# Kernel optimization log

Measured on AMD Instinct MI355X. Metric: run time of the kernel, lower is better.

The kernel has to match this reference:

```python
import jax, jax.numpy as jnp
import numpy as np

EPS = 1e-6
N, D = 8192, 256


def setup_inputs() -> dict:
    key = jax.random.key(0)
    kq, kc = jax.random.split(key)
    # scale 0.05 keeps points inside the Poincare ball: c*||q||^2 ~ 0.06 << 1
    query = jax.random.normal(kq, (N, D), dtype=jnp.float32) * 0.05
    c = jnp.asarray(0.1, dtype=jnp.float32)  # learnable curvature param (init 0.1)
    return {"query": query, "c": c}


def reference(query, c):
    # Self-attention path of HyperbolicAttention (keys = values = query).
    clamp_c = jnp.maximum(c, EPS)
    # ||u-v||^2 = ||u||^2 + ||v||^2 - 2 u.v  (same math as explicit expand+subtract,
    # but via a single GEMM instead of an (N, N, D) intermediate)
    qn = jnp.sum(query * query, axis=-1)                       # (N,)
    gram = query @ query.T                                     # (N, N)
    diff_sq = jnp.maximum(qn[:, None] + qn[None, :] - 2.0 * gram, 0.0)
    t = jnp.maximum(1.0 - clamp_c * qn, EPS)                   # clamped 1 - c||x||^2
    denom = t[:, None] * t[None, :]                            # (N, N)
    arg = jnp.maximum(1.0 + 2.0 * clamp_c * diff_sq / denom, 1.0 + EPS) + EPS
    dist = jnp.arccosh(arg) / jnp.sqrt(clamp_c)                # (N, N)
    attn = jax.nn.softmax(-dist, axis=-1)                      # (N, N)
    return attn @ query                                        # (N, D)
```

## Files before the change

### kernel.cpp

```cpp
#include <hip/hip_runtime.h>
#include <math.h>

#define NN 8192
#define DD 256
#define EPSV 1e-6f
#define BM 32
#define BN 256
#define NJT (NN / BN)
#define TSTR 266

typedef __bf16 bf16x8 __attribute__((ext_vector_type(8)));
typedef float f32x16 __attribute__((ext_vector_type(16)));
typedef unsigned short ushort;
typedef unsigned int uint;


__device__ inline ushort f2bf(float x) {
    uint u = __float_as_uint(x);
    u += 0x7fffu + ((u >> 16) & 1u);
    return (ushort)(u >> 16);
}

__global__ void prep_kernel(const float* __restrict__ q, const float* __restrict__ cp,
                            ushort* __restrict__ qbfA, ushort* __restrict__ qbfB,
                            float2* __restrict__ qni) {
    __shared__ ushort T[64 * TSTR];
    const int t = threadIdx.x;
    const int b = blockIdx.x;
    const int pr = t >> 2, fq = t & 3;
    const int row = b * 64 + pr;
    const float4* src = (const float4*)(q + (size_t)row * DD + fq * 64);
    ushort loc[64];
    float ss = 0.f;
    #pragma unroll
    for (int i = 0; i < 16; ++i) {
        float4 v = src[i];
        ushort b0 = f2bf(v.x), b1 = f2bf(v.y), b2 = f2bf(v.z), b3 = f2bf(v.w);
        loc[i * 4 + 0] = b0; loc[i * 4 + 1] = b1; loc[i * 4 + 2] = b2; loc[i * 4 + 3] = b3;
        float r0 = __uint_as_float((uint)b0 << 16), r1 = __uint_as_float((uint)b1 << 16);
        float r2 = __uint_as_float((uint)b2 << 16), r3 = __uint_as_float((uint)b3 << 16);
        ss += r0 * r0 + r1 * r1 + r2 * r2 + r3 * r3;
    }
    #pragma unroll
    for (int k = 0; k < 8; ++k)
        *(uint4*)(qbfA + (((size_t)b * 32 + fq * 8 + k) * 64 + pr) * 8) = *(uint4*)&loc[k * 8];
    #pragma unroll
    for (int k = 0; k < 32; ++k)
        *(ushort2*)&T[pr * TSTR + fq * 64 + k * 2] = *(ushort2*)&loc[k * 2];
    ss += __shfl_xor(ss, 1, 64);
    ss += __shfl_xor(ss, 2, 64);
    if (fq == 0) {
        float cc = fmaxf(cp[0], EPSV);
        float tt = fmaxf(1.0f - cc * ss, EPSV);
        qni[row] = make_float2(ss, sqrtf(2.0f * cc) / tt);
    }
    __syncthreads();
    #pragma unroll
    for (int pass = 0; pass < 4; ++pass) {
        int f = pass * 64 + (t >> 2);
        int quarter = t & 3;
        ushort tmp[16];
        #pragma unroll
        for (int i = 0; i < 16; ++i) tmp[i] = T[(quarter * 16 + i) * TSTR + f];
        *(uint4*)(qbfB + (((size_t)b * 8 + quarter * 2 + 0) * 256 + f) * 8) = *(uint4*)&tmp[0];
        *(uint4*)(qbfB + (((size_t)b * 8 + quarter * 2 + 1) * 256 + f) * 8) = *(uint4*)&tmp[8];
    }
}

__global__ __launch_bounds__(512, 2) void flash_kernel(
    const ushort* __restrict__ qbfA, const ushort* __restrict__ qbfB,
    const float* __restrict__ cp, const float2* __restrict__ qni,
    float* __restrict__ out) {
    __shared__ char px[32768];
    __shared__ float lrow[32];

    const int tid = threadIdx.x;
    const int lane = tid & 63;
    const int w = tid >> 6;
    const int l31 = lane & 31;
    const int lhi = lane >> 5;
    const int bx = blockIdx.x;
    const int R0 = bx * 32;

    if (tid < 32) lrow[tid] = 0.f;

    const float cc = fmaxf(cp[0], EPSV);
    const float nrsc = -rsqrtf(cc);

    bf16x8 qa[16];
    {
        const int jbQ = bx >> 1;
        const int rl = (bx & 1) * 32 + l31;
        #pragma unroll
        for (int kk = 0; kk < 16; ++kk)
            qa[kk] = *(const bf16x8*)(qbfA + (((size_t)jbQ * 32 + kk * 2 + lhi) * 64 + rl) * 8);
    }
    const float2 mv = qni[R0 + l31];
    const float qn_m = mv.x, itv_m = mv.y;

    f32x16 o;
    #pragma unroll
    for (int i = 0; i < 16; ++i) o[i] = 0.f;
    float racc = 0.f;

    #pragma unroll 1
    for (int jt = 0; jt < NJT; ++jt) {
        const int J0 = jt * BN;

        const int jbK = jt * 4 + (w >> 1);
        const int rlK = (w & 1) * 32 + l31;
        f32x16 s;
        #pragma unroll
        for (int i = 0; i < 16; ++i) s[i] = 0.f;
        #pragma unroll
        for (int kk = 0; kk < 16; ++kk) {
            bf16x8 kb = *(const bf16x8*)(qbfA + (((size_t)jbK * 32 + kk * 2 + lhi) * 64 + rlK) * 8);
            s = __builtin_amdgcn_mfma_f32_32x32x16_bf16(kb, qa[kk], s, 0, 0, 0);
        }

        float qnj[16], itj[16];
        #pragma unroll
        for (int rq = 0; rq < 4; ++rq) {
            int j0 = J0 + w * 32 + rq * 8 + 4 * lhi;
            const float4* qp = (const float4*)(qni + j0);
            float4 q01 = qp[0], q23 = qp[1];
            qnj[rq * 4 + 0] = q01.x; itj[rq * 4 + 0] = q01.y;
            qnj[rq * 4 + 1] = q01.z; itj[rq * 4 + 1] = q01.w;
            qnj[rq * 4 + 2] = q23.x; itj[rq * 4 + 2] = q23.y;
            qnj[rq * 4 + 3] = q23.z; itj[rq * 4 + 3] = q23.w;
        }

        float p[16];
        #pragma unroll
        for (int r = 0; r < 16; ++r) {
            float diff = fmaf(-2.0f, s[r], qn_m + qnj[r]);
            float z = fmaf(diff, itv_m * itj[r], 1.0f);
            z = fmaxf(z, 1.0f + EPSV) + EPSV;
            float y = z + sqrtf(fmaf(z, z, -1.0f));
            float pv = __builtin_amdgcn_exp2f(nrsc * __builtin_amdgcn_logf(y));
            racc += pv;
            p[r] = pv;
        }

        float sh[16];
        #pragma unroll
        for (int r = 0; r < 16; ++r) sh[r] = __shfl_xor(p[r], 32, 64);
        bf16x8 af0, af1;
        #pragma unroll
        for (int e = 0; e < 4; ++e) {
            af0[e]     = (__bf16)(lhi ? sh[e + 4]  : p[e]);
            af0[e + 4] = (__bf16)(lhi ? p[e + 4]  : sh[e]);
            af1[e]     = (__bf16)(lhi ? sh[e + 12] : p[e + 8]);
            af1[e + 4] = (__bf16)(lhi ? p[e + 12] : sh[e + 8]);
        }

        char* pxb = px + (jt & 1) * 16384;
        *(bf16x8*)(pxb + (w * 2 + 0) * 1024 + lane * 16) = af0;
        *(bf16x8*)(pxb + (w * 2 + 1) * 1024 + lane * 16) = af1;
        __syncthreads();

        #pragma unroll
        for (int kc = 0; kc < 16; ++kc) {
            bf16x8 pa = *(const bf16x8*)(pxb + kc * 1024 + lane * 16);
            bf16x8 vb = *(const bf16x8*)(qbfB +
                (((size_t)(jt * 16 + kc) * 2 + lhi) * 256 + w * 32 + l31) * 8);
            o = __builtin_amdgcn_mfma_f32_32x32x16_bf16(pa, vb, o, 0, 0, 0);
        }
    }

    racc += __shfl_xor(racc, 32, 64);
    if (lhi == 0) atomicAdd(&lrow[l31], racc);
    __syncthreads();
    #pragma unroll
    for (int r = 0; r < 16; ++r) {
        int row = (r & 3) + 8 * (r >> 2) + 4 * lhi;
        float inv = 1.0f / lrow[row];
        out[(size_t)(R0 + row) * DD + w * 32 + l31] = o[r] * inv;
    }
}

extern "C" void kernel_launch(void* const* d_in, const int* in_sizes, int n_in,
                              void* d_out, int out_size, void* d_ws, size_t ws_size,
                              hipStream_t stream) {
    (void)in_sizes; (void)n_in; (void)out_size; (void)ws_size;
    const float* q = (const float*)d_in[0];
    const float* cp = (const float*)d_in[1];
    float* out = (float*)d_out;
    float* ws = (float*)d_ws;
    float2* qni = (float2*)ws;
    ushort* qbfA = (ushort*)(qni + NN);
    ushort* qbfB = qbfA + (size_t)NN * DD;

    prep_kernel<<<NN / 64, 256, 0, stream>>>(q, cp, qbfA, qbfB, qni);
    flash_kernel<<<NN / BM, 512, 0, stream>>>(qbfA, qbfB, cp, qni, out);
}
```

Measured before the change: 255.7 us.

## Split key dimension across four blocks per row tile with separate normalize kernel

Each row tile's key range is partitioned into four chunks processed by separate blocks. Each block writes its unnormalized output and row sums to workspace, and a new reduction kernel sums them and divides. This is meant to fix underutilization, since there were only 256 blocks before, and launch bounds are raised to allow more blocks per CU. In exchange it adds extra global traffic for the partial results, and the tighter register budget risks spills.

```diff
diff --git a/kernel.cpp b/kernel.cpp
--- a/kernel.cpp
+++ b/kernel.cpp
@@ -6,7 +6,8 @@
 #define EPSV 1e-6f
 #define BM 32
 #define BN 256
-#define NJT (NN / BN)
+#define CSPLIT 4
+#define NJT (NN / CSPLIT / BN)
 #define TSTR 266
 
 typedef __bf16 bf16x8 __attribute__((ext_vector_type(8)));
@@ -67,10 +68,10 @@
     }
 }
 
-__global__ __launch_bounds__(512, 2) void flash_kernel(
+__global__ __launch_bounds__(512, 4) void flash_kernel(
     const ushort* __restrict__ qbfA, const ushort* __restrict__ qbfB,
     const float* __restrict__ cp, const float2* __restrict__ qni,
-    float* __restrict__ out) {
+    float* __restrict__ Oacc, float* __restrict__ lacc) {
     __shared__ char px[32768];
     __shared__ float lrow[32];
 
@@ -79,8 +80,9 @@
     const int w = tid >> 6;
     const int l31 = lane & 31;
     const int lhi = lane >> 5;
-    const int bx = blockIdx.x;
-    const int R0 = bx * 32;
+    const int cs = blockIdx.x & 3;
+    const int rb = blockIdx.x >> 2;
+    const int R0 = rb * BM;
 
     if (tid < 32) lrow[tid] = 0.f;
 
@@ -89,8 +91,8 @@
 
     bf16x8 qa[16];
     {
-        const int jbQ = bx >> 1;
-        const int rl = (bx & 1) * 32 + l31;
+        const int jbQ = rb >> 1;
+        const int rl = (rb & 1) * 32 + l31;
         #pragma unroll
         for (int kk = 0; kk < 16; ++kk)
             qa[kk] = *(const bf16x8*)(qbfA + (((size_t)jbQ * 32 + kk * 2 + lhi) * 64 + rl) * 8);
@@ -105,9 +107,9 @@
 
     #pragma unroll 1
     for (int jt = 0; jt < NJT; ++jt) {
-        const int J0 = jt * BN;
-
-        const int jbK = jt * 4 + (w >> 1);
+        const int J0 = cs * (NN / CSPLIT) + jt * BN;
+
+        const int jbK = (J0 >> 6) + (w >> 1);
         const int rlK = (w & 1) * 32 + l31;
         f32x16 s;
         #pragma unroll
@@ -159,11 +161,12 @@
         *(bf16x8*)(pxb + (w * 2 + 1) * 1024 + lane * 16) = af1;
         __syncthreads();
 
+        const size_t vslot0 = (size_t)(J0 >> 3);
         #pragma unroll
         for (int kc = 0; kc < 16; ++kc) {
             bf16x8 pa = *(const bf16x8*)(pxb + kc * 1024 + lane * 16);
             bf16x8 vb = *(const bf16x8*)(qbfB +
-                (((size_t)(jt * 16 + kc) * 2 + lhi) * 256 + w * 32 + l31) * 8);
+                ((vslot0 + kc * 2 + lhi) * 256 + w * 32 + l31) * 8);
             o = __builtin_amdgcn_mfma_f32_32x32x16_bf16(pa, vb, o, 0, 0, 0);
         }
     }
@@ -171,12 +174,32 @@
     racc += __shfl_xor(racc, 32, 64);
     if (lhi == 0) atomicAdd(&lrow[l31], racc);
     __syncthreads();
+    float* Oslab = Oacc + (size_t)cs * NN * DD;
     #pragma unroll
     for (int r = 0; r < 16; ++r) {
         int row = (r & 3) + 8 * (r >> 2) + 4 * lhi;
-        float inv = 1.0f / lrow[row];
-        out[(size_t)(R0 + row) * DD + w * 32 + l31] = o[r] * inv;
-    }
+        Oslab[(size_t)(R0 + row) * DD + w * 32 + l31] = o[r];
+    }
+    if (tid < 32) lacc[cs * NN + R0 + tid] = lrow[tid];
+}
+
+__global__ void norm_kernel(const float* __restrict__ Oacc, const float* __restrict__ lacc,
+                            float* __restrict__ out) {
+    int i = blockIdx.x * 256 + threadIdx.x;
+    int row = i >> 6;
+    float l = lacc[row] + lacc[NN + row] + lacc[2 * NN + row] + lacc[3 * NN + row];
+    const size_t stride = (size_t)NN * DD / 4;
+    float4 a = ((const float4*)Oacc)[i];
+    float4 b = ((const float4*)Oacc)[i + stride];
+    float4 c = ((const float4*)Oacc)[i + 2 * stride];
+    float4 d = ((const float4*)Oacc)[i + 3 * stride];
+    float inv = 1.0f / l;
+    float4 r;
+    r.x = (a.x + b.x + c.x + d.x) * inv;
+    r.y = (a.y + b.y + c.y + d.y) * inv;
+    r.z = (a.z + b.z + c.z + d.z) * inv;
+    r.w = (a.w + b.w + c.w + d.w) * inv;
+    ((float4*)out)[i] = r;
 }
 
 extern "C" void kernel_launch(void* const* d_in, const int* in_sizes, int n_in,
@@ -190,7 +213,10 @@
     float2* qni = (float2*)ws;
     ushort* qbfA = (ushort*)(qni + NN);
     ushort* qbfB = qbfA + (size_t)NN * DD;
+    float* lacc = (float*)(qbfB + (size_t)NN * DD);
+    float* Oacc = lacc + CSPLIT * NN;
 
     prep_kernel<<<NN / 64, 256, 0, stream>>>(q, cp, qbfA, qbfB, qni);
-    flash_kernel<<<NN / BM, 512, 0, stream>>>(qbfA, qbfB, cp, qni, out);
-}
+    flash_kernel<<<CSPLIT * (NN / BM), 512, 0, stream>>>(qbfA, qbfB, cp, qni, Oacc, lacc);
+    norm_kernel<<<NN * DD / 4 / 256, 256, 0, stream>>>(Oacc, lacc, out);
+}
```

Result: slower. 352.4 us (+37.8%).
